# Optimization experiments

Measured on AMD Instinct MI355X. Metric: run time of the kernel, lower is better.

The kernel has to match this reference:

```python
import jax, jax.numpy as jnp
import numpy as np

N = 100000      # nodes
E = 3200000     # edges (avg degree 32)
F_IN = 256      # input features
HID = 16        # ARMA hidden width (hard-coded in Net)
C = 16          # num classes
K = 2           # ARMA stacks


def _arma_conv(x, src, dst, init_w, root_w, bias, act):
    """ARMAConv with num_layers=1, shared_weights=True (eval mode, no dropout).
    x: [N, F_in]; init_w/root_w: [K, F_in, F_out]; bias: [K, F_out].
    Returns [N, F_out] (mean over K stacks)."""
    n = x.shape[0]
    # gcn_norm with add_self_loops=False: deg from target (col) index
    deg = jax.ops.segment_sum(jnp.ones_like(src, jnp.float32), dst, num_segments=n)
    dinv = jnp.where(deg > 0, jax.lax.rsqrt(jnp.maximum(deg, 1.0)), 0.0)
    norm = dinv[src] * dinv[dst]                      # [E]
    h = jnp.einsum('nf,kfo->nko', x, init_w)          # [N, K, F_out]
    msg = h[src] * norm[:, None, None]                # [E, K, F_out]
    agg = jax.ops.segment_sum(msg, dst, num_segments=n)  # [N, K, F_out]
    root = jnp.einsum('nf,kfo->nko', x, root_w)       # [N, K, F_out]
    out = act(agg + root + bias[None])                # [N, K, F_out]
    return out.mean(axis=1)                           # [N, F_out]


def setup_inputs() -> dict:
    key = jax.random.key(0)
    ks = jax.random.split(key, 8)
    x = jax.random.normal(ks[0], (N, F_IN), jnp.float32)
    edge_index = jax.random.randint(ks[1], (2, E), 0, N, dtype=jnp.int64)
    s1 = 1.0 / np.sqrt(F_IN)
    s2 = 1.0 / np.sqrt(HID)
    return {
        'x': x,
        'edge_index': edge_index,
        'init_w1': jax.random.normal(ks[2], (K, F_IN, HID), jnp.float32) * s1,
        'root_w1': jax.random.normal(ks[3], (K, F_IN, HID), jnp.float32) * s1,
        'bias1':   jnp.zeros((K, HID), jnp.float32),
        'init_w2': jax.random.normal(ks[4], (K, HID, C), jnp.float32) * s2,
        'root_w2': jax.random.normal(ks[5], (K, HID, C), jnp.float32) * s2,
        'bias2':   jnp.zeros((K, C), jnp.float32),
    }


def reference(x, edge_index, init_w1, root_w1, bias1, init_w2, root_w2, bias2):
    src, dst = edge_index[0], edge_index[1]
    # conv1 uses internal ReLU (ARMAConv default act); Net applies F.relu again
    h = jax.nn.relu(_arma_conv(x, src, dst, init_w1, root_w1, bias1, jax.nn.relu))
    agg_feature = h                                    # detached copy in original
    logits = _arma_conv(h, src, dst, init_w2, root_w2, bias2, lambda t: t)
    return jax.nn.log_softmax(logits, axis=1), agg_feature
```

## Files before the change

kernel.cpp:

```cpp
#include <hip/hip_runtime.h>
#include <cstdint>
#include <cstddef>

#define N_NODES 100000
#define N_EDGES 3200000
#define F_IN    256
#define HID     16
#define KH      32
#define C_OUT   16

#define W_LOG   7
#define W       128
#define NBKT    782
#define CAP     4608
#define EPB     4096

typedef short  bf16x8 __attribute__((ext_vector_type(8)));
typedef float  f32x4  __attribute__((ext_vector_type(4)));
typedef unsigned short u16x8 __attribute__((ext_vector_type(8)));

__device__ __forceinline__ unsigned short f2bf(float f) {
    uint32_t u = __builtin_bit_cast(uint32_t, f);
    u += 0x7fffu + ((u >> 16) & 1u);
    return (unsigned short)(u >> 16);
}
__device__ __forceinline__ float bf2f(unsigned short s) {
    return __builtin_bit_cast(float, (uint32_t)s << 16);
}

__global__ __launch_bounds__(256) void k_part(const int* __restrict__ src,
                                              const int* __restrict__ dst,
                                              int* __restrict__ gcur,
                                              unsigned int* __restrict__ bucketed) {
    __shared__ int hist[NBKT];
    __shared__ int lcur[NBKT];
    __shared__ unsigned int pbuf[EPB];
    __shared__ unsigned short bbuf[EPB];
    int tid = threadIdx.x;
    for (int i = tid; i < NBKT; i += 256) hist[i] = 0;
    __syncthreads();
    int e0 = blockIdx.x * EPB;
    int cnt = min(EPB, N_EDGES - e0);
    for (int i = tid; i < cnt; i += 256) {
        int s = src[e0 + i], d = dst[e0 + i];
        int b = d >> W_LOG;
        pbuf[i] = ((unsigned int)s << W_LOG) | (unsigned int)(d & (W - 1));
        bbuf[i] = (unsigned short)b;
        atomicAdd(&hist[b], 1);
    }
    __syncthreads();
    for (int b = tid; b < NBKT; b += 256) {
        int h = hist[b];
        lcur[b] = h > 0 ? atomicAdd(&gcur[b], h) : 0;
    }
    __syncthreads();
    for (int i = tid; i < cnt; i += 256) {
        int b = bbuf[i];
        int pos = atomicAdd(&lcur[b], 1);
        if (pos < CAP) bucketed[(size_t)b * CAP + pos] = pbuf[i];
    }
}

__global__ __launch_bounds__(256) void k_sort(const unsigned int* __restrict__ bucketed,
                                              const int* __restrict__ gcur,
                                              int* __restrict__ sorted,
                                              int2* __restrict__ meta,
                                              float* __restrict__ dinv) {
    __shared__ int hist[W], pre[W], cur[W];
    __shared__ int sbuf[CAP];
    int tid = threadIdx.x, b = blockIdx.x;
    int cnt = min(gcur[b], CAP);
    const unsigned int* bp = bucketed + (size_t)b * CAP;
    if (tid < W) hist[tid] = 0;
    __syncthreads();
    for (int i = tid; i < cnt; i += 256) atomicAdd(&hist[bp[i] & (W - 1)], 1);
    __syncthreads();
    if (tid < W) pre[tid] = hist[tid];
    __syncthreads();
    for (int off = 1; off < W; off <<= 1) {
        int v = (tid < W && tid >= off) ? pre[tid - off] : 0;
        __syncthreads();
        if (tid < W) pre[tid] += v;
        __syncthreads();
    }
    if (tid < W) cur[tid] = pre[tid] - hist[tid];
    __syncthreads();
    for (int i = tid; i < cnt; i += 256) {
        unsigned int p = bp[i];
        int pos = atomicAdd(&cur[p & (W - 1)], 1);
        sbuf[pos] = (int)(p >> W_LOG);
    }
    __syncthreads();
    int* so = sorted + (size_t)b * CAP;
    for (int i = tid; i < cnt; i += 256) so[i] = sbuf[i];
    int node = b * W + tid;
    if (tid < W && node < N_NODES) {
        int h = hist[tid];
        meta[node] = make_int2(b * CAP + (pre[tid] - h), h);
        dinv[node] = h > 0 ? rsqrtf((float)h) : 0.f;
    }
}

__global__ __launch_bounds__(512) void k_gemm1(
    const float* __restrict__ x, const float* __restrict__ wi,
    const float* __restrict__ wr, const float* __restrict__ dinv,
    unsigned short* __restrict__ h1c, float* __restrict__ r1) {
    __shared__ unsigned short wt[64 * 256];
    int tid = threadIdx.x;

    for (int i = tid; i < 8192; i += 512) {
        int ksk = i >> 12, f = (i >> 4) & 255, o = i & 15;
        int col = ksk * 16 + o;
        int slot = (f >> 3) ^ (col & 7);
        wt[col * 256 + slot * 8 + (f & 7)] = f2bf(wi[i]);
    }
    for (int i = tid; i < 8192; i += 512) {
        int ksk = i >> 12, f = (i >> 4) & 255, o = i & 15;
        int col = 32 + ksk * 16 + o;
        int slot = (f >> 3) ^ (col & 7);
        wt[col * 256 + slot * 8 + (f & 7)] = f2bf(wr[i]);
    }
    __syncthreads();

    int lane = tid & 63;
    int wv   = tid >> 6;
    int base = blockIdx.x * 128 + wv * 16;
    int row16 = lane & 15;
    int akg   = lane >> 4;
    int gr = min(base + row16, N_NODES - 1);
    const float* xp = x + (size_t)gr * F_IN + akg * 8;

    f32x4 acc[4] = {{0, 0, 0, 0}, {0, 0, 0, 0}, {0, 0, 0, 0}, {0, 0, 0, 0}};

    #pragma unroll
    for (int ks = 0; ks < 8; ++ks) {
        float4 v0 = *reinterpret_cast<const float4*>(xp + ks * 32);
        float4 v1 = *reinterpret_cast<const float4*>(xp + ks * 32 + 4);
        u16x8 p;
        p[0] = f2bf(v0.x); p[1] = f2bf(v0.y); p[2] = f2bf(v0.z); p[3] = f2bf(v0.w);
        p[4] = f2bf(v1.x); p[5] = f2bf(v1.y); p[6] = f2bf(v1.z); p[7] = f2bf(v1.w);
        bf16x8 af = __builtin_bit_cast(bf16x8, p);
        #pragma unroll
        for (int c = 0; c < 4; ++c) {
            int col = c * 16 + row16;
            int slot = (ks * 4 + akg) ^ (col & 7);
            bf16x8 bfr = *reinterpret_cast<const bf16x8*>(&wt[col * 256 + slot * 8]);
            acc[c] = __builtin_amdgcn_mfma_f32_16x16x32_bf16(af, bfr, acc[c], 0, 0, 0);
        }
    }

    float dv[4];
    #pragma unroll
    for (int r = 0; r < 4; ++r) {
        int n = base + (lane >> 4) * 4 + r;
        dv[r] = (n < N_NODES) ? dinv[n] : 0.f;
    }
    #pragma unroll
    for (int c = 0; c < 4; ++c) {
        #pragma unroll
        for (int r = 0; r < 4; ++r) {
            int n = base + (lane >> 4) * 4 + r;
            if (n < N_NODES) {
                int col = c * 16 + row16;
                float v = acc[c][r];
                if (col < KH) h1c[(size_t)n * KH + col] = f2bf(v * dv[r]);
                else          r1[(size_t)n * KH + (col - KH)] = v;
            }
        }
    }
}

__global__ __launch_bounds__(512) void k_gath1p(
    const int* __restrict__ sorted, const int2* __restrict__ meta,
    const float* __restrict__ dinv, const unsigned short* __restrict__ h1c,
    const float* __restrict__ r1, const float* __restrict__ b1,
    const float* __restrict__ wi2, const float* __restrict__ wr2,
    float* __restrict__ hout, unsigned short* __restrict__ h2t,
    float* __restrict__ r2m) {
    __shared__ float wm[512];
    int tid = threadIdx.x;
    if (tid < 256)      wm[tid] = 0.5f * (wi2[tid] + wi2[256 + tid]);
    else                wm[tid] = 0.5f * (wr2[tid - 256] + wr2[256 + tid - 256]);
    __syncthreads();

    int t = blockIdx.x * 512 + tid;
    int n = t >> 3, q = t & 7;
    if (n >= N_NODES) return;
    int2 m = meta[n];
    const int* sp = sorted + m.x;
    float ax = 0, ay = 0, az = 0, aw = 0;
    int j = 0;
    for (; j + 4 <= m.y; j += 4) {
        int s0 = sp[j], s1 = sp[j + 1], s2 = sp[j + 2], s3 = sp[j + 3];
        ushort4 v0 = *reinterpret_cast<const ushort4*>(h1c + (size_t)s0 * KH + q * 4);
        ushort4 v1 = *reinterpret_cast<const ushort4*>(h1c + (size_t)s1 * KH + q * 4);
        ushort4 v2 = *reinterpret_cast<const ushort4*>(h1c + (size_t)s2 * KH + q * 4);
        ushort4 v3 = *reinterpret_cast<const ushort4*>(h1c + (size_t)s3 * KH + q * 4);
        ax += (bf2f(v0.x) + bf2f(v1.x)) + (bf2f(v2.x) + bf2f(v3.x));
        ay += (bf2f(v0.y) + bf2f(v1.y)) + (bf2f(v2.y) + bf2f(v3.y));
        az += (bf2f(v0.z) + bf2f(v1.z)) + (bf2f(v2.z) + bf2f(v3.z));
        aw += (bf2f(v0.w) + bf2f(v1.w)) + (bf2f(v2.w) + bf2f(v3.w));
    }
    for (; j < m.y; ++j) {
        int s0 = sp[j];
        ushort4 v0 = *reinterpret_cast<const ushort4*>(h1c + (size_t)s0 * KH + q * 4);
        ax += bf2f(v0.x); ay += bf2f(v0.y); az += bf2f(v0.z); aw += bf2f(v0.w);
    }
    float dn = dinv[n];
    float4 rv = *reinterpret_cast<const float4*>(r1 + (size_t)n * KH + q * 4);
    float zi[4];
    zi[0] = fmaxf(ax * dn + rv.x + b1[q * 4 + 0], 0.f);
    zi[1] = fmaxf(ay * dn + rv.y + b1[q * 4 + 1], 0.f);
    zi[2] = fmaxf(az * dn + rv.z + b1[q * 4 + 2], 0.f);
    zi[3] = fmaxf(aw * dn + rv.w + b1[q * 4 + 3], 0.f);
    float h4[4];
    #pragma unroll
    for (int i = 0; i < 4; ++i)
        h4[i] = 0.5f * (zi[i] + __shfl_xor(zi[i], 4));
    if (q < 4)
        *reinterpret_cast<float4*>(hout + (size_t)n * HID + q * 4) =
            make_float4(h4[0], h4[1], h4[2], h4[3]);
    int lane = tid & 63;
    int bl = lane & 56;
    float hf[16];
    #pragma unroll
    for (int jj = 0; jj < 4; ++jj)
        #pragma unroll
        for (int i = 0; i < 4; ++i)
            hf[jj * 4 + i] = __shfl(h4[i], bl + jj);
    const float* wsel = (q < 4) ? wm : wm + 256;
    int ocb = (q & 3) * 4;
    float o4[4] = {0, 0, 0, 0};
    #pragma unroll
    for (int k = 0; k < HID; ++k) {
        float hv = hf[k];
        o4[0] += hv * wsel[k * 16 + ocb + 0];
        o4[1] += hv * wsel[k * 16 + ocb + 1];
        o4[2] += hv * wsel[k * 16 + ocb + 2];
        o4[3] += hv * wsel[k * 16 + ocb + 3];
    }
    if (q < 4) {
        ushort4 hw;
        hw.x = f2bf(o4[0] * dn); hw.y = f2bf(o4[1] * dn);
        hw.z = f2bf(o4[2] * dn); hw.w = f2bf(o4[3] * dn);
        *reinterpret_cast<ushort4*>(h2t + (size_t)n * HID + ocb) = hw;
    } else {
        *reinterpret_cast<float4*>(r2m + (size_t)n * HID + ocb) =
            make_float4(o4[0], o4[1], o4[2], o4[3]);
    }
}

__global__ __launch_bounds__(256) void k_gath2p(
    const int* __restrict__ sorted, const int2* __restrict__ meta,
    const float* __restrict__ dinv, const unsigned short* __restrict__ h2t,
    const float* __restrict__ r2m, const float* __restrict__ b2,
    float* __restrict__ out) {
    int t = blockIdx.x * 256 + threadIdx.x;
    int n = t >> 2, q = t & 3;
    if (n >= N_NODES) return;
    int2 m = meta[n];
    const int* sp = sorted + m.x;
    float ax = 0, ay = 0, az = 0, aw = 0;
    int j = 0;
    for (; j + 4 <= m.y; j += 4) {
        int s0 = sp[j], s1 = sp[j + 1], s2 = sp[j + 2], s3 = sp[j + 3];
        ushort4 v0 = *reinterpret_cast<const ushort4*>(h2t + (size_t)s0 * HID + q * 4);
        ushort4 v1 = *reinterpret_cast<const ushort4*>(h2t + (size_t)s1 * HID + q * 4);
        ushort4 v2 = *reinterpret_cast<const ushort4*>(h2t + (size_t)s2 * HID + q * 4);
        ushort4 v3 = *reinterpret_cast<const ushort4*>(h2t + (size_t)s3 * HID + q * 4);
        ax += (bf2f(v0.x) + bf2f(v1.x)) + (bf2f(v2.x) + bf2f(v3.x));
        ay += (bf2f(v0.y) + bf2f(v1.y)) + (bf2f(v2.y) + bf2f(v3.y));
        az += (bf2f(v0.z) + bf2f(v1.z)) + (bf2f(v2.z) + bf2f(v3.z));
        aw += (bf2f(v0.w) + bf2f(v1.w)) + (bf2f(v2.w) + bf2f(v3.w));
    }
    for (; j < m.y; ++j) {
        int s0 = sp[j];
        ushort4 v0 = *reinterpret_cast<const ushort4*>(h2t + (size_t)s0 * HID + q * 4);
        ax += bf2f(v0.x); ay += bf2f(v0.y); az += bf2f(v0.z); aw += bf2f(v0.w);
    }
    float dn = dinv[n];
    float4 rv = *reinterpret_cast<const float4*>(r2m + (size_t)n * HID + q * 4);
    float z[4];
    z[0] = ax * dn + rv.x + 0.5f * (b2[q * 4 + 0] + b2[16 + q * 4 + 0]);
    z[1] = ay * dn + rv.y + 0.5f * (b2[q * 4 + 1] + b2[16 + q * 4 + 1]);
    z[2] = az * dn + rv.z + 0.5f * (b2[q * 4 + 2] + b2[16 + q * 4 + 2]);
    z[3] = aw * dn + rv.w + 0.5f * (b2[q * 4 + 3] + b2[16 + q * 4 + 3]);
    float lm = fmaxf(fmaxf(z[0], z[1]), fmaxf(z[2], z[3]));
    lm = fmaxf(lm, __shfl_xor(lm, 1));
    float mx = fmaxf(lm, __shfl_xor(lm, 2));
    float sl = expf(z[0] - mx) + expf(z[1] - mx) + expf(z[2] - mx) + expf(z[3] - mx);
    sl += __shfl_xor(sl, 1);
    float s = sl + __shfl_xor(sl, 2);
    float ls = logf(s);
    *reinterpret_cast<float4*>(out + (size_t)n * C_OUT + q * 4) =
        make_float4(z[0] - mx - ls, z[1] - mx - ls, z[2] - mx - ls, z[3] - mx - ls);
}

extern "C" void kernel_launch(void* const* d_in, const int* in_sizes, int n_in,
                              void* d_out, int out_size, void* d_ws, size_t ws_size,
                              hipStream_t stream) {
    const float* x   = (const float*)d_in[0];
    const int*   ei  = (const int*)d_in[1];
    const float* wi1 = (const float*)d_in[2];
    const float* wr1 = (const float*)d_in[3];
    const float* b1  = (const float*)d_in[4];
    const float* wi2 = (const float*)d_in[5];
    const float* wr2 = (const float*)d_in[6];
    const float* b2  = (const float*)d_in[7];
    float* out = (float*)d_out;

    int* gcur = (int*)d_ws;
    unsigned int* bucketed = (unsigned int*)(gcur + 1024);
    int* sorted = (int*)(bucketed + (size_t)NBKT * CAP);
    int2* meta  = (int2*)(sorted + (size_t)NBKT * CAP);
    float* dinv = (float*)(meta + N_NODES);
    float* r1   = dinv + N_NODES;
    float* r2m  = r1 + (size_t)N_NODES * KH;
    unsigned short* h1c = (unsigned short*)(r2m + (size_t)N_NODES * HID);
    unsigned short* h2t = h1c + (size_t)N_NODES * KH;

    const int* srcI = ei;
    const int* dstI = ei + N_EDGES;

    hipMemsetAsync(gcur, 0, 1024 * sizeof(int), stream);

    k_part<<<(N_EDGES + EPB - 1) / EPB, 256, 0, stream>>>(srcI, dstI, gcur, bucketed);
    k_sort<<<NBKT, 256, 0, stream>>>(bucketed, gcur, sorted, meta, dinv);
    k_gemm1<<<(N_NODES + 127) / 128, 512, 0, stream>>>(x, wi1, wr1, dinv, h1c, r1);
    k_gath1p<<<(N_NODES * 8 + 511) / 512, 512, 0, stream>>>(
        sorted, meta, dinv, h1c, r1, b1, wi2, wr2,
        out + (size_t)N_NODES * C_OUT, h2t, r2m);
    k_gath2p<<<(N_NODES * 4 + 255) / 256, 256, 0, stream>>>(
        sorted, meta, dinv, h2t, r2m, b2, out);
}
```

Measured before the change: 331.7 us.

## Fuse partition with GEMM1, defer dinv scaling to sort, widen gather vectors

Partitioning and the first GEMM now run in one launch, split by block index over a union of shared-memory layouts, so the two independent stages can overlap on the GPU. Because the GEMM no longer waits for degrees, the dinv row scaling of h1c moves into the sort kernel as a bf16 read-modify-write. The root terms r1 and r2m are stored as bf16 instead of fp32. Both gather kernels now use 16-byte vector loads with fewer threads per node. This adds an extra pass over h1c and a second bf16 rounding, which lowers precision.

```diff
diff --git a/kernel.cpp b/kernel.cpp
--- a/kernel.cpp
+++ b/kernel.cpp
@@ -14,6 +14,8 @@
 #define NBKT    782
 #define CAP     4608
 #define EPB     4096
+#define PART_BLOCKS 782
+#define GEMM_BLOCKS 782
 
 typedef short  bf16x8 __attribute__((ext_vector_type(8)));
 typedef float  f32x4  __attribute__((ext_vector_type(4)));
@@ -28,103 +30,71 @@
     return __builtin_bit_cast(float, (uint32_t)s << 16);
 }
 
-__global__ __launch_bounds__(256) void k_part(const int* __restrict__ src,
-                                              const int* __restrict__ dst,
-                                              int* __restrict__ gcur,
-                                              unsigned int* __restrict__ bucketed) {
-    __shared__ int hist[NBKT];
-    __shared__ int lcur[NBKT];
-    __shared__ unsigned int pbuf[EPB];
-    __shared__ unsigned short bbuf[EPB];
+struct PartSmem {
+    int hist[NBKT];
+    int lcur[NBKT];
+    unsigned int pbuf[EPB];
+    unsigned short bbuf[EPB];
+};
+struct GemmSmem {
+    unsigned short wt[64 * 256];
+};
+union FusedSmem { PartSmem p; GemmSmem g; };
+
+__global__ __launch_bounds__(512) void k_partgemm(
+    const int* __restrict__ src, const int* __restrict__ dst,
+    int* __restrict__ gcur, unsigned int* __restrict__ bucketed,
+    const float* __restrict__ x, const float* __restrict__ wi,
+    const float* __restrict__ wr, const float* __restrict__ dinv_unused,
+    unsigned short* __restrict__ h1c, unsigned short* __restrict__ r1b) {
+    __shared__ FusedSmem sm;
     int tid = threadIdx.x;
-    for (int i = tid; i < NBKT; i += 256) hist[i] = 0;
-    __syncthreads();
-    int e0 = blockIdx.x * EPB;
-    int cnt = min(EPB, N_EDGES - e0);
-    for (int i = tid; i < cnt; i += 256) {
-        int s = src[e0 + i], d = dst[e0 + i];
-        int b = d >> W_LOG;
-        pbuf[i] = ((unsigned int)s << W_LOG) | (unsigned int)(d & (W - 1));
-        bbuf[i] = (unsigned short)b;
-        atomicAdd(&hist[b], 1);
-    }
-    __syncthreads();
-    for (int b = tid; b < NBKT; b += 256) {
-        int h = hist[b];
-        lcur[b] = h > 0 ? atomicAdd(&gcur[b], h) : 0;
-    }
-    __syncthreads();
-    for (int i = tid; i < cnt; i += 256) {
-        int b = bbuf[i];
-        int pos = atomicAdd(&lcur[b], 1);
-        if (pos < CAP) bucketed[(size_t)b * CAP + pos] = pbuf[i];
-    }
-}
-
-__global__ __launch_bounds__(256) void k_sort(const unsigned int* __restrict__ bucketed,
-                                              const int* __restrict__ gcur,
-                                              int* __restrict__ sorted,
-                                              int2* __restrict__ meta,
-                                              float* __restrict__ dinv) {
-    __shared__ int hist[W], pre[W], cur[W];
-    __shared__ int sbuf[CAP];
-    int tid = threadIdx.x, b = blockIdx.x;
-    int cnt = min(gcur[b], CAP);
-    const unsigned int* bp = bucketed + (size_t)b * CAP;
-    if (tid < W) hist[tid] = 0;
-    __syncthreads();
-    for (int i = tid; i < cnt; i += 256) atomicAdd(&hist[bp[i] & (W - 1)], 1);
-    __syncthreads();
-    if (tid < W) pre[tid] = hist[tid];
-    __syncthreads();
-    for (int off = 1; off < W; off <<= 1) {
-        int v = (tid < W && tid >= off) ? pre[tid - off] : 0;
-        __syncthreads();
-        if (tid < W) pre[tid] += v;
-        __syncthreads();
-    }
-    if (tid < W) cur[tid] = pre[tid] - hist[tid];
-    __syncthreads();
-    for (int i = tid; i < cnt; i += 256) {
-        unsigned int p = bp[i];
-        int pos = atomicAdd(&cur[p & (W - 1)], 1);
-        sbuf[pos] = (int)(p >> W_LOG);
-    }
-    __syncthreads();
-    int* so = sorted + (size_t)b * CAP;
-    for (int i = tid; i < cnt; i += 256) so[i] = sbuf[i];
-    int node = b * W + tid;
-    if (tid < W && node < N_NODES) {
-        int h = hist[tid];
-        meta[node] = make_int2(b * CAP + (pre[tid] - h), h);
-        dinv[node] = h > 0 ? rsqrtf((float)h) : 0.f;
-    }
-}
-
-__global__ __launch_bounds__(512) void k_gemm1(
-    const float* __restrict__ x, const float* __restrict__ wi,
-    const float* __restrict__ wr, const float* __restrict__ dinv,
-    unsigned short* __restrict__ h1c, float* __restrict__ r1) {
-    __shared__ unsigned short wt[64 * 256];
-    int tid = threadIdx.x;
-
+
+    if (blockIdx.x < PART_BLOCKS) {
+        int pb = blockIdx.x;
+        for (int i = tid; i < NBKT; i += 512) sm.p.hist[i] = 0;
+        __syncthreads();
+        int e0 = pb * EPB;
+        int cnt = min(EPB, N_EDGES - e0);
+        for (int i = tid; i < cnt; i += 512) {
+            int s = src[e0 + i], d = dst[e0 + i];
+            int b = d >> W_LOG;
+            sm.p.pbuf[i] = ((unsigned int)s << W_LOG) | (unsigned int)(d & (W - 1));
+            sm.p.bbuf[i] = (unsigned short)b;
+            atomicAdd(&sm.p.hist[b], 1);
+        }
+        __syncthreads();
+        for (int b = tid; b < NBKT; b += 512) {
+            int h = sm.p.hist[b];
+            sm.p.lcur[b] = h > 0 ? atomicAdd(&gcur[b], h) : 0;
+        }
+        __syncthreads();
+        for (int i = tid; i < cnt; i += 512) {
+            int b = sm.p.bbuf[i];
+            int pos = atomicAdd(&sm.p.lcur[b], 1);
+            if (pos < CAP) bucketed[(size_t)b * CAP + pos] = sm.p.pbuf[i];
+        }
+        return;
+    }
+
+    int gb = blockIdx.x - PART_BLOCKS;
     for (int i = tid; i < 8192; i += 512) {
         int ksk = i >> 12, f = (i >> 4) & 255, o = i & 15;
         int col = ksk * 16 + o;
         int slot = (f >> 3) ^ (col & 7);
-        wt[col * 256 + slot * 8 + (f & 7)] = f2bf(wi[i]);
+        sm.g.wt[col * 256 + slot * 8 + (f & 7)] = f2bf(wi[i]);
     }
     for (int i = tid; i < 8192; i += 512) {
         int ksk = i >> 12, f = (i >> 4) & 255, o = i & 15;
         int col = 32 + ksk * 16 + o;
         int slot = (f >> 3) ^ (col & 7);
-        wt[col * 256 + slot * 8 + (f & 7)] = f2bf(wr[i]);
+        sm.g.wt[col * 256 + slot * 8 + (f & 7)] = f2bf(wr[i]);
     }
     __syncthreads();
 
     int lane = tid & 63;
     int wv   = tid >> 6;
-    int base = blockIdx.x * 128 + wv * 16;
+    int base = gb * 128 + wv * 16;
     int row16 = lane & 15;
     int akg   = lane >> 4;
     int gr = min(base + row16, N_NODES - 1);
@@ -144,17 +114,11 @@
         for (int c = 0; c < 4; ++c) {
             int col = c * 16 + row16;
             int slot = (ks * 4 + akg) ^ (col & 7);
-            bf16x8 bfr = *reinterpret_cast<const bf16x8*>(&wt[col * 256 + slot * 8]);
+            bf16x8 bfr = *reinterpret_cast<const bf16x8*>(&sm.g.wt[col * 256 + slot * 8]);
             acc[c] = __builtin_amdgcn_mfma_f32_16x16x32_bf16(af, bfr, acc[c], 0, 0, 0);
         }
     }
 
-    float dv[4];
-    #pragma unroll
-    for (int r = 0; r < 4; ++r) {
-        int n = base + (lane >> 4) * 4 + r;
-        dv[r] = (n < N_NODES) ? dinv[n] : 0.f;
-    }
     #pragma unroll
     for (int c = 0; c < 4; ++c) {
         #pragma unroll
@@ -163,9 +127,67 @@
             if (n < N_NODES) {
                 int col = c * 16 + row16;
                 float v = acc[c][r];
-                if (col < KH) h1c[(size_t)n * KH + col] = f2bf(v * dv[r]);
-                else          r1[(size_t)n * KH + (col - KH)] = v;
+                if (col < KH) h1c[(size_t)n * KH + col] = f2bf(v);
+                else          r1b[(size_t)n * KH + (col - KH)] = f2bf(v);
             }
+        }
+    }
+}
+
+__global__ __launch_bounds__(256) void k_sort(const unsigned int* __restrict__ bucketed,
+                                              const int* __restrict__ gcur,
+                                              int* __restrict__ sorted,
+                                              int2* __restrict__ meta,
+                                              float* __restrict__ dinv,
+                                              unsigned short* __restrict__ h1c) {
+    __shared__ int hist[W], pre[W], cur[W];
+    __shared__ int sbuf[CAP];
+    int tid = threadIdx.x, b = blockIdx.x;
+    int cnt = min(gcur[b], CAP);
+    const unsigned int* bp = bucketed + (size_t)b * CAP;
+    if (tid < W) hist[tid] = 0;
+    __syncthreads();
+    for (int i = tid; i < cnt; i += 256) atomicAdd(&hist[bp[i] & (W - 1)], 1);
+    __syncthreads();
+    if (tid < W) pre[tid] = hist[tid];
+    __syncthreads();
+    for (int off = 1; off < W; off <<= 1) {
+        int v = (tid < W && tid >= off) ? pre[tid - off] : 0;
+        __syncthreads();
+        if (tid < W) pre[tid] += v;
+        __syncthreads();
+    }
+    if (tid < W) cur[tid] = pre[tid] - hist[tid];
+    __syncthreads();
+    for (int i = tid; i < cnt; i += 256) {
+        unsigned int p = bp[i];
+        int pos = atomicAdd(&cur[p & (W - 1)], 1);
+        sbuf[pos] = (int)(p >> W_LOG);
+    }
+    __syncthreads();
+    int* so = sorted + (size_t)b * CAP;
+    for (int i = tid; i < cnt; i += 256) so[i] = sbuf[i];
+    int node = b * W + tid;
+    float dv = 0.f;
+    if (tid < W && node < N_NODES) {
+        int h = hist[tid];
+        meta[node] = make_int2(b * CAP + (pre[tid] - h), h);
+        dv = h > 0 ? rsqrtf((float)h) : 0.f;
+        dinv[node] = dv;
+    }
+    __syncthreads();
+    int rn = b * W + (tid >> 1);
+    if (rn < N_NODES) {
+        float d2 = (tid & 1) ? hist[0] : 0.f;
+        (void)d2;
+        float dr = dinv[rn];
+        u16x8* row = reinterpret_cast<u16x8*>(h1c + (size_t)rn * KH + (tid & 1) * 16);
+        #pragma unroll
+        for (int g = 0; g < 2; ++g) {
+            u16x8 v = row[g];
+            #pragma unroll
+            for (int i = 0; i < 8; ++i) v[i] = f2bf(bf2f(v[i]) * dr);
+            row[g] = v;
         }
     }
 }
@@ -173,127 +195,133 @@
 __global__ __launch_bounds__(512) void k_gath1p(
     const int* __restrict__ sorted, const int2* __restrict__ meta,
     const float* __restrict__ dinv, const unsigned short* __restrict__ h1c,
-    const float* __restrict__ r1, const float* __restrict__ b1,
+    const unsigned short* __restrict__ r1b, const float* __restrict__ b1,
     const float* __restrict__ wi2, const float* __restrict__ wr2,
     float* __restrict__ hout, unsigned short* __restrict__ h2t,
-    float* __restrict__ r2m) {
+    unsigned short* __restrict__ r2mb) {
     __shared__ float wm[512];
+    __shared__ float sb1[32];
     int tid = threadIdx.x;
     if (tid < 256)      wm[tid] = 0.5f * (wi2[tid] + wi2[256 + tid]);
-    else                wm[tid] = 0.5f * (wr2[tid - 256] + wr2[256 + tid - 256]);
+    else                wm[tid] = 0.5f * (wr2[tid - 256] + wr2[tid]);
+    if (tid < 32) sb1[tid] = b1[tid];
     __syncthreads();
 
     int t = blockIdx.x * 512 + tid;
-    int n = t >> 3, q = t & 7;
-    if (n >= N_NODES) return;
-    int2 m = meta[n];
-    const int* sp = sorted + m.x;
-    float ax = 0, ay = 0, az = 0, aw = 0;
-    int j = 0;
-    for (; j + 4 <= m.y; j += 4) {
-        int s0 = sp[j], s1 = sp[j + 1], s2 = sp[j + 2], s3 = sp[j + 3];
-        ushort4 v0 = *reinterpret_cast<const ushort4*>(h1c + (size_t)s0 * KH + q * 4);
-        ushort4 v1 = *reinterpret_cast<const ushort4*>(h1c + (size_t)s1 * KH + q * 4);
-        ushort4 v2 = *reinterpret_cast<const ushort4*>(h1c + (size_t)s2 * KH + q * 4);
-        ushort4 v3 = *reinterpret_cast<const ushort4*>(h1c + (size_t)s3 * KH + q * 4);
-        ax += (bf2f(v0.x) + bf2f(v1.x)) + (bf2f(v2.x) + bf2f(v3.x));
-        ay += (bf2f(v0.y) + bf2f(v1.y)) + (bf2f(v2.y) + bf2f(v3.y));
-        az += (bf2f(v0.z) + bf2f(v1.z)) + (bf2f(v2.z) + bf2f(v3.z));
-        aw += (bf2f(v0.w) + bf2f(v1.w)) + (bf2f(v2.w) + bf2f(v3.w));
-    }
-    for (; j < m.y; ++j) {
-        int s0 = sp[j];
-        ushort4 v0 = *reinterpret_cast<const ushort4*>(h1c + (size_t)s0 * KH + q * 4);
-        ax += bf2f(v0.x); ay += bf2f(v0.y); az += bf2f(v0.z); aw += bf2f(v0.w);
-    }
-    float dn = dinv[n];
-    float4 rv = *reinterpret_cast<const float4*>(r1 + (size_t)n * KH + q * 4);
-    float zi[4];
-    zi[0] = fmaxf(ax * dn + rv.x + b1[q * 4 + 0], 0.f);
-    zi[1] = fmaxf(ay * dn + rv.y + b1[q * 4 + 1], 0.f);
-    zi[2] = fmaxf(az * dn + rv.z + b1[q * 4 + 2], 0.f);
-    zi[3] = fmaxf(aw * dn + rv.w + b1[q * 4 + 3], 0.f);
-    float h4[4];
-    #pragma unroll
-    for (int i = 0; i < 4; ++i)
-        h4[i] = 0.5f * (zi[i] + __shfl_xor(zi[i], 4));
-    if (q < 4)
-        *reinterpret_cast<float4*>(hout + (size_t)n * HID + q * 4) =
-            make_float4(h4[0], h4[1], h4[2], h4[3]);
-    int lane = tid & 63;
-    int bl = lane & 56;
-    float hf[16];
-    #pragma unroll
-    for (int jj = 0; jj < 4; ++jj)
-        #pragma unroll
-        for (int i = 0; i < 4; ++i)
-            hf[jj * 4 + i] = __shfl(h4[i], bl + jj);
-    const float* wsel = (q < 4) ? wm : wm + 256;
-    int ocb = (q & 3) * 4;
-    float o4[4] = {0, 0, 0, 0};
-    #pragma unroll
-    for (int k = 0; k < HID; ++k) {
-        float hv = hf[k];
-        o4[0] += hv * wsel[k * 16 + ocb + 0];
-        o4[1] += hv * wsel[k * 16 + ocb + 1];
-        o4[2] += hv * wsel[k * 16 + ocb + 2];
-        o4[3] += hv * wsel[k * 16 + ocb + 3];
-    }
-    if (q < 4) {
-        ushort4 hw;
-        hw.x = f2bf(o4[0] * dn); hw.y = f2bf(o4[1] * dn);
-        hw.z = f2bf(o4[2] * dn); hw.w = f2bf(o4[3] * dn);
-        *reinterpret_cast<ushort4*>(h2t + (size_t)n * HID + ocb) = hw;
-    } else {
-        *reinterpret_cast<float4*>(r2m + (size_t)n * HID + ocb) =
-            make_float4(o4[0], o4[1], o4[2], o4[3]);
-    }
-}
-
-__global__ __launch_bounds__(256) void k_gath2p(
-    const int* __restrict__ sorted, const int2* __restrict__ meta,
-    const float* __restrict__ dinv, const unsigned short* __restrict__ h2t,
-    const float* __restrict__ r2m, const float* __restrict__ b2,
-    float* __restrict__ out) {
-    int t = blockIdx.x * 256 + threadIdx.x;
     int n = t >> 2, q = t & 3;
     if (n >= N_NODES) return;
     int2 m = meta[n];
     const int* sp = sorted + m.x;
-    float ax = 0, ay = 0, az = 0, aw = 0;
+    float a[8] = {0, 0, 0, 0, 0, 0, 0, 0};
     int j = 0;
     for (; j + 4 <= m.y; j += 4) {
         int s0 = sp[j], s1 = sp[j + 1], s2 = sp[j + 2], s3 = sp[j + 3];
-        ushort4 v0 = *reinterpret_cast<const ushort4*>(h2t + (size_t)s0 * HID + q * 4);
-        ushort4 v1 = *reinterpret_cast<const ushort4*>(h2t + (size_t)s1 * HID + q * 4);
-        ushort4 v2 = *reinterpret_cast<const ushort4*>(h2t + (size_t)s2 * HID + q * 4);
-        ushort4 v3 = *reinterpret_cast<const ushort4*>(h2t + (size_t)s3 * HID + q * 4);
-        ax += (bf2f(v0.x) + bf2f(v1.x)) + (bf2f(v2.x) + bf2f(v3.x));
-        ay += (bf2f(v0.y) + bf2f(v1.y)) + (bf2f(v2.y) + bf2f(v3.y));
-        az += (bf2f(v0.z) + bf2f(v1.z)) + (bf2f(v2.z) + bf2f(v3.z));
-        aw += (bf2f(v0.w) + bf2f(v1.w)) + (bf2f(v2.w) + bf2f(v3.w));
+        u16x8 v0 = *reinterpret_cast<const u16x8*>(h1c + (size_t)s0 * KH + q * 8);
+        u16x8 v1 = *reinterpret_cast<const u16x8*>(h1c + (size_t)s1 * KH + q * 8);
+        u16x8 v2 = *reinterpret_cast<const u16x8*>(h1c + (size_t)s2 * KH + q * 8);
+        u16x8 v3 = *reinterpret_cast<const u16x8*>(h1c + (size_t)s3 * KH + q * 8);
+        #pragma unroll
+        for (int i = 0; i < 8; ++i)
+            a[i] += (bf2f(v0[i]) + bf2f(v1[i])) + (bf2f(v2[i]) + bf2f(v3[i]));
     }
     for (; j < m.y; ++j) {
         int s0 = sp[j];
-        ushort4 v0 = *reinterpret_cast<const ushort4*>(h2t + (size_t)s0 * HID + q * 4);
-        ax += bf2f(v0.x); ay += bf2f(v0.y); az += bf2f(v0.z); aw += bf2f(v0.w);
+        u16x8 v0 = *reinterpret_cast<const u16x8*>(h1c + (size_t)s0 * KH + q * 8);
+        #pragma unroll
+        for (int i = 0; i < 8; ++i) a[i] += bf2f(v0[i]);
     }
     float dn = dinv[n];
-    float4 rv = *reinterpret_cast<const float4*>(r2m + (size_t)n * HID + q * 4);
-    float z[4];
-    z[0] = ax * dn + rv.x + 0.5f * (b2[q * 4 + 0] + b2[16 + q * 4 + 0]);
-    z[1] = ay * dn + rv.y + 0.5f * (b2[q * 4 + 1] + b2[16 + q * 4 + 1]);
-    z[2] = az * dn + rv.z + 0.5f * (b2[q * 4 + 2] + b2[16 + q * 4 + 2]);
-    z[3] = aw * dn + rv.w + 0.5f * (b2[q * 4 + 3] + b2[16 + q * 4 + 3]);
-    float lm = fmaxf(fmaxf(z[0], z[1]), fmaxf(z[2], z[3]));
-    lm = fmaxf(lm, __shfl_xor(lm, 1));
-    float mx = fmaxf(lm, __shfl_xor(lm, 2));
-    float sl = expf(z[0] - mx) + expf(z[1] - mx) + expf(z[2] - mx) + expf(z[3] - mx);
-    sl += __shfl_xor(sl, 1);
-    float s = sl + __shfl_xor(sl, 2);
+    u16x8 rt = *reinterpret_cast<const u16x8*>(r1b + (size_t)n * KH + q * 8);
+    float h8[8];
+    #pragma unroll
+    for (int i = 0; i < 8; ++i) {
+        float zi = fmaxf(a[i] * dn + bf2f(rt[i]) + sb1[q * 8 + i], 0.f);
+        h8[i] = zi;
+    }
+    #pragma unroll
+    for (int i = 0; i < 8; ++i)
+        h8[i] = 0.5f * (h8[i] + __shfl_xor(h8[i], 2));
+    if (q < 2) {
+        float4* ho = reinterpret_cast<float4*>(hout + (size_t)n * HID + q * 8);
+        ho[0] = make_float4(h8[0], h8[1], h8[2], h8[3]);
+        ho[1] = make_float4(h8[4], h8[5], h8[6], h8[7]);
+    }
+    int lane = tid & 63;
+    int bl = lane & 60;
+    float hf[16];
+    #pragma unroll
+    for (int kk = 0; kk < 8; ++kk) {
+        hf[kk]     = __shfl(h8[kk], bl);
+        hf[8 + kk] = __shfl(h8[kk], bl + 1);
+    }
+    const float* wsel = (q < 2) ? wm : wm + 256;
+    int ocb = (q & 1) * 8;
+    float o8[8] = {0, 0, 0, 0, 0, 0, 0, 0};
+    #pragma unroll
+    for (int k = 0; k < HID; ++k) {
+        float hv = hf[k];
+        #pragma unroll
+        for (int i = 0; i < 8; ++i) o8[i] += hv * wsel[k * 16 + ocb + i];
+    }
+    u16x8 wv8;
+    if (q < 2) {
+        #pragma unroll
+        for (int i = 0; i < 8; ++i) wv8[i] = f2bf(o8[i] * dn);
+        *reinterpret_cast<u16x8*>(h2t + (size_t)n * HID + ocb) = wv8;
+    } else {
+        #pragma unroll
+        for (int i = 0; i < 8; ++i) wv8[i] = f2bf(o8[i]);
+        *reinterpret_cast<u16x8*>(r2mb + (size_t)n * HID + ocb) = wv8;
+    }
+}
+
+__global__ __launch_bounds__(256) void k_gath2p(
+    const int* __restrict__ sorted, const int2* __restrict__ meta,
+    const float* __restrict__ dinv, const unsigned short* __restrict__ h2t,
+    const unsigned short* __restrict__ r2mb, const float* __restrict__ b2,
+    float* __restrict__ out) {
+    int t = blockIdx.x * 256 + threadIdx.x;
+    int n = t >> 1, q = t & 1;
+    if (n >= N_NODES) return;
+    int2 m = meta[n];
+    const int* sp = sorted + m.x;
+    float a[8] = {0, 0, 0, 0, 0, 0, 0, 0};
+    int j = 0;
+    for (; j + 4 <= m.y; j += 4) {
+        int s0 = sp[j], s1 = sp[j + 1], s2 = sp[j + 2], s3 = sp[j + 3];
+        u16x8 v0 = *reinterpret_cast<const u16x8*>(h2t + (size_t)s0 * HID + q * 8);
+        u16x8 v1 = *reinterpret_cast<const u16x8*>(h2t + (size_t)s1 * HID + q * 8);
+        u16x8 v2 = *reinterpret_cast<const u16x8*>(h2t + (size_t)s2 * HID + q * 8);
+        u16x8 v3 = *reinterpret_cast<const u16x8*>(h2t + (size_t)s3 * HID + q * 8);
+        #pragma unroll
+        for (int i = 0; i < 8; ++i)
+            a[i] += (bf2f(v0[i]) + bf2f(v1[i])) + (bf2f(v2[i]) + bf2f(v3[i]));
+    }
+    for (; j < m.y; ++j) {
+        int s0 = sp[j];
+        u16x8 v0 = *reinterpret_cast<const u16x8*>(h2t + (size_t)s0 * HID + q * 8);
+        #pragma unroll
+        for (int i = 0; i < 8; ++i) a[i] += bf2f(v0[i]);
+    }
+    float dn = dinv[n];
+    u16x8 rt = *reinterpret_cast<const u16x8*>(r2mb + (size_t)n * HID + q * 8);
+    float z[8];
+    float lm = -1e30f;
+    #pragma unroll
+    for (int i = 0; i < 8; ++i) {
+        int c = q * 8 + i;
+        z[i] = a[i] * dn + bf2f(rt[i]) + 0.5f * (b2[c] + b2[16 + c]);
+        lm = fmaxf(lm, z[i]);
+    }
+    float mx = fmaxf(lm, __shfl_xor(lm, 1));
+    float sl = 0.f;
+    #pragma unroll
+    for (int i = 0; i < 8; ++i) sl += expf(z[i] - mx);
+    float s = sl + __shfl_xor(sl, 1);
     float ls = logf(s);
-    *reinterpret_cast<float4*>(out + (size_t)n * C_OUT + q * 4) =
-        make_float4(z[0] - mx - ls, z[1] - mx - ls, z[2] - mx - ls, z[3] - mx - ls);
+    float4* o4 = reinterpret_cast<float4*>(out + (size_t)n * C_OUT + q * 8);
+    o4[0] = make_float4(z[0] - mx - ls, z[1] - mx - ls, z[2] - mx - ls, z[3] - mx - ls);
+    o4[1] = make_float4(z[4] - mx - ls, z[5] - mx - ls, z[6] - mx - ls, z[7] - mx - ls);
 }
 
 extern "C" void kernel_launch(void* const* d_in, const int* in_sizes, int n_in,
@@ -314,22 +342,22 @@
     int* sorted = (int*)(bucketed + (size_t)NBKT * CAP);
     int2* meta  = (int2*)(sorted + (size_t)NBKT * CAP);
     float* dinv = (float*)(meta + N_NODES);
-    float* r1   = dinv + N_NODES;
-    float* r2m  = r1 + (size_t)N_NODES * KH;
-    unsigned short* h1c = (unsigned short*)(r2m + (size_t)N_NODES * HID);
-    unsigned short* h2t = h1c + (size_t)N_NODES * KH;
+    unsigned short* h1c  = (unsigned short*)(dinv + N_NODES);
+    unsigned short* h2t  = h1c + (size_t)N_NODES * KH;
+    unsigned short* r1b  = h2t + (size_t)N_NODES * HID;
+    unsigned short* r2mb = r1b + (size_t)N_NODES * KH;
 
     const int* srcI = ei;
     const int* dstI = ei + N_EDGES;
 
     hipMemsetAsync(gcur, 0, 1024 * sizeof(int), stream);
 
-    k_part<<<(N_EDGES + EPB - 1) / EPB, 256, 0, stream>>>(srcI, dstI, gcur, bucketed);
-    k_sort<<<NBKT, 256, 0, stream>>>(bucketed, gcur, sorted, meta, dinv);
-    k_gemm1<<<(N_NODES + 127) / 128, 512, 0, stream>>>(x, wi1, wr1, dinv, h1c, r1);
-    k_gath1p<<<(N_NODES * 8 + 511) / 512, 512, 0, stream>>>(
-        sorted, meta, dinv, h1c, r1, b1, wi2, wr2,
-        out + (size_t)N_NODES * C_OUT, h2t, r2m);
-    k_gath2p<<<(N_NODES * 4 + 255) / 256, 256, 0, stream>>>(
-        sorted, meta, dinv, h2t, r2m, b2, out);
-}
+    k_partgemm<<<PART_BLOCKS + GEMM_BLOCKS, 512, 0, stream>>>(
+        srcI, dstI, gcur, bucketed, x, wi1, wr1, nullptr, h1c, r1b);
+    k_sort<<<NBKT, 256, 0, stream>>>(bucketed, gcur, sorted, meta, dinv, h1c);
+    k_gath1p<<<(N_NODES * 4 + 511) / 512, 512, 0, stream>>>(
+        sorted, meta, dinv, h1c, r1b, b1, wi2, wr2,
+        out + (size_t)N_NODES * C_OUT, h2t, r2mb);
+    k_gath2p<<<(N_NODES * 2 + 255) / 256, 256, 0, stream>>>(
+        sorted, meta, dinv, h2t, r2mb, b2, out);
+}
```

Result: faster. 312.5 us (-5.8%).
